# Performance work log

Measured on AMD Instinct MI355X. Metric: run time of the kernel, lower is better.

The kernel has to match this reference:

```python
import jax, jax.numpy as jnp
import numpy as np
import math

B, HR, WR, C = 8, 128, 128, 192
WS, SS = 8, 4
NH, SPH, CHH = 8, 6, 2
DH = C // NH  # 24
AREA = WS * WS
MID = max(C // 4, 8)
NWIN = (HR // WS) * (WR // WS)
LOGMAX = math.log(100.0)

def _rel_pos_index(ws):
    coords = np.stack(np.meshgrid(np.arange(ws), np.arange(ws), indexing='ij')).reshape(2, -1)
    rel = (coords[:, :, None] - coords[:, None, :]).transpose(1, 2, 0).copy()
    rel[:, :, 0] += ws - 1
    rel[:, :, 1] += ws - 1
    rel[:, :, 0] *= 2 * ws - 1
    return rel.sum(-1)  # (AREA, AREA)

def _attn_mask(H, W, ws, ss):
    img = np.zeros((H, W))
    sl = (slice(0, -ws), slice(-ws, -ss), slice(-ss, None))
    cnt = 0
    for hs in sl:
        for wsl in sl:
            img[hs, wsl] = cnt
            cnt += 1
    mw = img.reshape(H // ws, ws, W // ws, ws).transpose(0, 2, 1, 3).reshape(-1, ws * ws)
    am = mw[:, None, :] - mw[:, :, None]
    return np.where(am != 0, -100.0, 0.0).astype(np.float32)

REL_IDX = jnp.asarray(_rel_pos_index(WS))
ATTN_MASK = jnp.asarray(_attn_mask(HR, WR, WS, SS))  # (NWIN, AREA, AREA)

def _norm(v):
    return v / jnp.maximum(jnp.linalg.norm(v, axis=-1, keepdims=True), 1e-12)

def _ln(x, g, b):
    m = x.mean(-1, keepdims=True)
    v = x.var(-1, keepdims=True)
    return (x - m) / jnp.sqrt(v + 1e-5) * g + b

def _bn(x, g, b, m, v):
    return (x - m) / jnp.sqrt(v + 1e-5) * g + b

def _conv3(x, w):  # x: NHWC, w: (O,I,3,3) torch layout
    return jax.lax.conv_general_dilated(x, jnp.transpose(w, (2, 3, 1, 0)), (1, 1), 'SAME', dimension_numbers=('NHWC', 'HWIO', 'NHWC'))

def _forward(x, ln1_g, ln1_b, w_qkv, b_qkv, logit_sp, rpb_table, w_spp, b_spp, logit_ch, w_chp, b_chp, w_sp_proj, w_ch_proj, w_s2c1, w_s2c2, b_s2c2, w_c2s1, w_c2s2, b_c2s2, w_gs1, w_gs2, b_gs2, w_gc1, w_gc2, b_gc2, w_f1, bn1_g, bn1_b, bn1_m, bn1_v, w_f2, bn2_g, bn2_b, bn2_m, bn2_v, w_sg1, w_sg2, b_sg2, ln2_g, ln2_b, w_fc1, b_fc1, w_fc2, b_fc2):
    h = _ln(x, ln1_g, ln1_b)
    img = h.reshape(B, HR, WR, C)
    # qkv conv1x1; per-head channel blocks of 3*DH (faithful to torch view)
    qkv = (img @ w_qkv.T + b_qkv).reshape(B, HR, WR, NH, 3 * DH)
    # ---- spatial shifted-window cosine attention (heads 0:SPH) ----
    sp = jnp.roll(qkv[..., :SPH, :], (-SS, -SS), axis=(1, 2))
    nHw, nWw = HR // WS, WR // WS
    sp = sp.reshape(B, nHw, WS, nWw, WS, SPH, 3 * DH).transpose(0, 1, 3, 5, 2, 4, 6)
    sp = sp.reshape(B * NWIN, SPH, AREA, 3 * DH)
    q, k, v = jnp.split(sp, 3, axis=-1)
    attn = jnp.einsum('bhid,bhjd->bhij', _norm(q), _norm(k))
    attn = attn * jnp.exp(jnp.minimum(logit_sp, LOGMAX)).reshape(1, SPH, 1, 1)
    attn = attn + rpb_table[REL_IDX].transpose(2, 0, 1)[None]
    attn = attn.reshape(B, NWIN, SPH, AREA, AREA) + ATTN_MASK[None, :, None]
    attn = jax.nn.softmax(attn.reshape(B * NWIN, SPH, AREA, AREA), axis=-1)
    o = jnp.einsum('bhij,bhjd->bhid', attn, v)
    o = o.reshape(B, nHw, nWw, SPH, WS, WS, DH).transpose(0, 1, 4, 2, 5, 3, 6).reshape(B, HR, WR, SPH * DH)
    o = o @ w_spp.T + b_spp
    sp_out = jnp.roll(o, (SS, SS), axis=(1, 2)) @ w_sp_proj.T  # (B,H,W,C)
    # ---- channel cosine self-attention (heads SPH:NH) ----
    chq = qkv[..., SPH:, :].reshape(B, HR * WR, CHH, 3 * DH).transpose(0, 2, 3, 1)  # (B,hh,3dh,HW)
    qc, kc, vc = jnp.split(chq, 3, axis=2)
    a = jnp.einsum('bhci,bhdi->bhcd', _norm(qc), _norm(kc))
    a = jax.nn.softmax(a * jnp.exp(jnp.minimum(logit_ch, LOGMAX)).reshape(1, CHH, 1, 1), axis=-1)
    oc = jnp.einsum('bhcd,bhdi->bhci', a, vc).reshape(B, CHH * DH, HR * WR)
    oc = oc.transpose(0, 2, 1).reshape(B, HR, WR, CHH * DH)
    ch_out = (oc @ w_chp.T + b_chp) @ w_ch_proj.T  # (B,H,W,C)
    # ---- CFCA cross gating ----
    def mlp1(t, w1, w2, b2):
        return jax.nn.relu(t @ w1.T) @ w2.T + b2
    sp2ch = mlp1(sp_out, w_s2c1, w_s2c2, b_s2c2) * jax.nn.sigmoid(mlp1(sp_out.mean((1, 2), keepdims=True), w_gs1, w_gs2, b_gs2))
    ch2sp = mlp1(ch_out, w_c2s1, w_c2s2, b_c2s2) * jax.nn.sigmoid(mlp1(ch_out.mean((1, 2), keepdims=True), w_gc1, w_gc2, b_gc2))
    spf = sp_out + ch2sp
    chf = ch_out + sp2ch
    # ---- XFF fusion (BN in eval mode) ----
    f = jnp.concatenate([spf, chf], axis=-1) @ w_f1.T
    f = jax.nn.relu(_bn(f, bn1_g, bn1_b, bn1_m, bn1_v))
    f = jax.nn.relu(_bn(_conv3(f, w_f2), bn2_g, bn2_b, bn2_m, bn2_v))
    g = jax.nn.sigmoid(jax.nn.relu(_conv3(f, w_sg1)) @ w_sg2.T + b_sg2)
    fused = f * g + f
    # ---- transformer block residual + MLP ----
    x = x + fused.reshape(B, HR * WR, C)
    h2 = _ln(x, ln2_g, ln2_b)
    return x + (jax.nn.gelu(h2 @ w_fc1.T + b_fc1, approximate=False) @ w_fc2.T + b_fc2)

def setup_inputs() -> dict:
    keys = iter(jax.random.split(jax.random.key(0), 64))
    def rn(shape, s=0.02):
        return jax.random.normal(next(keys), shape, dtype=jnp.float32) * s
    z = lambda *s: jnp.zeros(s, dtype=jnp.float32)
    o = lambda *s: jnp.ones(s, dtype=jnp.float32)
    return {
        'x': jax.random.normal(next(keys), (B, HR * WR, C), dtype=jnp.float32),
        'ln1_g': o(C), 'ln1_b': z(C),
        'w_qkv': rn((3 * C, C)), 'b_qkv': z(3 * C),
        'logit_sp': jnp.full((SPH,), math.log(10.0), dtype=jnp.float32),
        'rpb_table': rn(((2 * WS - 1) ** 2, SPH)),
        'w_spp': rn((SPH * DH, SPH * DH)), 'b_spp': z(SPH * DH),
        'logit_ch': jnp.full((CHH,), math.log(10.0), dtype=jnp.float32),
        'w_chp': rn((CHH * DH, CHH * DH)), 'b_chp': z(CHH * DH),
        'w_sp_proj': rn((C, SPH * DH)), 'w_ch_proj': rn((C, CHH * DH)),
        'w_s2c1': rn((MID, C)), 'w_s2c2': rn((C, MID)), 'b_s2c2': z(C),
        'w_c2s1': rn((MID, C)), 'w_c2s2': rn((C, MID)), 'b_c2s2': z(C),
        'w_gs1': rn((MID, C)), 'w_gs2': rn((C, MID)), 'b_gs2': z(C),
        'w_gc1': rn((MID, C)), 'w_gc2': rn((C, MID)), 'b_gc2': z(C),
        'w_f1': rn((C, 2 * C)),
        'bn1_g': o(C), 'bn1_b': z(C), 'bn1_m': z(C), 'bn1_v': o(C),
        'w_f2': rn((C, C, 3, 3)),
        'bn2_g': o(C), 'bn2_b': z(C), 'bn2_m': z(C), 'bn2_v': o(C),
        'w_sg1': rn((C // 2, C, 3, 3)), 'w_sg2': rn((1, C // 2)), 'b_sg2': z(1),
        'ln2_g': o(C), 'ln2_b': z(C),
        'w_fc1': rn((4 * C, C)), 'b_fc1': z(4 * C), 'w_fc2': rn((C, 4 * C)), 'b_fc2': z(C),
    }

def reference(x, ln1_g, ln1_b, w_qkv, b_qkv, logit_sp, rpb_table, w_spp, b_spp, logit_ch, w_chp, b_chp, w_sp_proj, w_ch_proj, w_s2c1, w_s2c2, b_s2c2, w_c2s1, w_c2s2, b_c2s2, w_gs1, w_gs2, b_gs2, w_gc1, w_gc2, b_gc2, w_f1, bn1_g, bn1_b, bn1_m, bn1_v, w_f2, bn2_g, bn2_b, bn2_m, bn2_v, w_sg1, w_sg2, b_sg2, ln2_g, ln2_b, w_fc1, b_fc1, w_fc2, b_fc2):
    return _forward(x, ln1_g, ln1_b, w_qkv, b_qkv, logit_sp, rpb_table, w_spp, b_spp, logit_ch, w_chp, b_chp, w_sp_proj, w_ch_proj, w_s2c1, w_s2c2, b_s2c2, w_c2s1, w_c2s2, b_c2s2, w_gs1, w_gs2, b_gs2, w_gc1, w_gc2, b_gc2, w_f1, bn1_g, bn1_b, bn1_m, bn1_v, w_f2, bn2_g, bn2_b, bn2_m, bn2_v, w_sg1, w_sg2, b_sg2, ln2_g, ln2_b, w_fc1, b_fc1, w_fc2, b_fc2)
```

## Files before the change

### kernel.cpp

```cpp
#include <hip/hip_runtime.h>
#include <hip/hip_bf16.h>
#include <cstddef>

typedef __hip_bfloat16 bf16;
typedef unsigned short u16;
typedef unsigned int u32;
typedef short s16x8 __attribute__((ext_vector_type(8)));
typedef float f32x4 __attribute__((ext_vector_type(4)));

#define BATCH 8
#define HR 128
#define WR 128
#define CCH 192
#define HW (HR*WR)
#define MTOK (BATCH*HW)
#define SPH 6
#define SPC 432
#define CHC 144
#define NWIN 256
#define MIDC 48
#define PH 130
#define PHW (PH*PH)
#define LOGMAX 4.6051701859880914f

static const size_t OFF_A0    = 0;
static const size_t OFF_B0    = 113246208;
static const size_t OFF_C0    = 150994944;
static const size_t OFF_SMALL = 188743680;
static const size_t SO_STATS  = 0;
static const size_t SO_PGRAM  = 1048576;
static const size_t SO_PSS    = 1638400;
static const size_t SO_ATTNB  = 1687552;
static const size_t SO_MEANSP = 1724416;
static const size_t SO_MEANCH = 1732608;
static const size_t SO_GATES  = 1740800;
static const size_t SO_GATEC  = 1748992;
static const size_t SO_BCSP   = 1757184;
static const size_t SO_WCCH   = 1758208;
static const size_t SO_BCCH   = 1795072;
static const size_t SO_WFUSE  = 1796096;
static const size_t SO_WCSPB  = 1943552;
static const size_t SO_WQB    = 1998848;
static const size_t SO_WS2C1B = 2220032;
static const size_t SO_WC2S1B = 2238464;
static const size_t SO_WS2C2B = 2256896;
static const size_t SO_WC2S2B = 2275328;
static const size_t SO_WF1B   = 2293760;
static const size_t SO_WF2CB  = 2441216;
static const size_t SO_WSG1CB = 3104768;
static const size_t SO_WFC1B  = 3436544;
static const size_t SO_WFC2B  = 3731456;

__device__ __forceinline__ float b2f(bf16 x) { return __bfloat162float(x); }
__device__ __forceinline__ bf16  f2b(float x){ return __float2bfloat16(x); }
__device__ __forceinline__ u16   f2u(float x){
    bf16 h = __float2bfloat16(x);
    union { bf16 b; u16 u; } c; c.b = h; return c.u;
}
__device__ __forceinline__ float s2f(short s){
    union { u16 u; bf16 b; } c; c.u = (u16)s; return b2f(c.b);
}
__device__ __forceinline__ float u2f(u16 u){
    union { u16 u; bf16 b; } c; c.u = u; return b2f(c.b);
}
__device__ __forceinline__ int xcdswz(int b, int n){
    const int q = n >> 3, r = n & 7, x = b & 7, o = b >> 3;
    return (x < r) ? (x * (q + 1) + o) : (r * (q + 1) + (x - r) * q + o);
}

#define GBM 128
#define GBK 32
#define LDA 40

struct SegRaw { union { uint4 v; struct { float4 lo, hi; } f; } d; };

template<int AMODE, int EPI, int CBF, int BNT, int CPAD, int WPB>
__global__ __launch_bounds__(256)
void gemm_k(const void* __restrict__ A, const u16* __restrict__ W,
            const float* __restrict__ bias, void* __restrict__ Cv,
            int M, int N, int K,
            const float* __restrict__ stats, const float* __restrict__ lng,
            const float* __restrict__ lnb, const void* __restrict__ A2,
            const float* __restrict__ ep0, const float* __restrict__ ep1,
            const float* __restrict__ ep2, const float* __restrict__ ep3)
{
    constexpr int NF = BNT / 32;
    constexpr int NB = (BNT * 4 + 255) / 256;
    constexpr int ATILE = GBM * LDA;
    constexpr int BTILE = BNT * LDA;
    constexpr int BUFSZ = ATILE + BTILE;
    constexpr int CST   = BNT + 8;
    __shared__ __align__(16) u16 smem[2 * BUFSZ];

    const int tid  = threadIdx.x;
    const int lane = tid & 63;
    const int wid  = tid >> 6;
    const int wm   = (wid >> 1) * 64;
    const int wn   = (wid & 1) * (BNT / 2);
    const int m0   = xcdswz(blockIdx.y, gridDim.y) * GBM;
    const int n0   = blockIdx.x * BNT;
    const int row16 = lane & 15;
    const int hi    = lane >> 4;
    const int koff  = hi * 8;

    const int arow[2] = { tid >> 2, (tid + 256) >> 2 };
    const int akk     = (tid & 3) * 8;

    const u16* Wb = W;
    if constexpr (WPB) Wb = W + (size_t)(m0 >> 14) * 9216;

    float meanA[2], rstdA[2];
    if constexpr (AMODE == 1) {
        #pragma unroll
        for (int it = 0; it < 2; ++it) {
            const int m = m0 + arow[it];
            meanA[it] = stats[2*m]; rstdA[it] = stats[2*m+1];
        }
    }

    f32x4 acc[4][NF];
    #pragma unroll
    for (int mf = 0; mf < 4; ++mf)
        #pragma unroll
        for (int nf = 0; nf < NF; ++nf)
            acc[mf][nf] = (f32x4){0.f, 0.f, 0.f, 0.f};

    const int nsteps = (K + GBK - 1) / GBK;

    auto loadA = [&](int step, SegRaw seg[2]) {
        const int k0 = step * GBK;
        #pragma unroll
        for (int it = 0; it < 2; ++it) {
            const int m = m0 + arow[it];
            const int k = k0 + akk;
            SegRaw& s = seg[it];
            if (k >= K) { s.d.v = (uint4){0u,0u,0u,0u}; continue; }
            if constexpr (AMODE == 0) {
                s.d.v = *(const uint4*)((const u16*)A + (size_t)m * K + k);
            } else if constexpr (AMODE == 1) {
                const float* p = (const float*)A + (size_t)m * K + k;
                s.d.f.lo = *(const float4*)p; s.d.f.hi = *(const float4*)(p+4);
            } else if constexpr (AMODE == 2) {
                const u16* src = (k < CCH) ? (const u16*)A  + (size_t)m * CCH + k
                                           : (const u16*)A2 + (size_t)m * CCH + (k - CCH);
                s.d.v = *(const uint4*)src;
            } else if constexpr (AMODE == 3) {
                const int tap = k / CCH, c = k - tap * CCH;
                const int ky = tap / 3, kx = tap - ky * 3;
                const int b = m >> 14, pix = m & 16383;
                const int h = pix >> 7, w = pix & 127;
                s.d.v = *(const uint4*)((const u16*)A +
                        ((size_t)b * PHW + (size_t)(h + ky) * PH + (w + kx)) * CCH + c);
            } else {
                const int col = (k < 24) ? (48 + k) : (96 + k);
                s.d.v = *(const uint4*)((const u16*)A + (size_t)m * CHC + col);
            }
        }
    };
    auto loadB = [&](int step, SegRaw seg[NB]) {
        const int k0 = step * GBK;
        #pragma unroll
        for (int it = 0; it < NB; ++it) {
            const int s = tid + it * 256;
            const int n = n0 + (s >> 2);
            const int k = k0 + (s & 3) * 8;
            seg[it].d.v = (uint4){0u,0u,0u,0u};
            if (s < BNT*4 && k < K && n < N)
                seg[it].d.v = *(const uint4*)(Wb + (size_t)n * K + k);
        }
    };
    auto writeA = [&](int step, SegRaw seg[2], u16* Ab) {
        const int k0 = step * GBK;
        #pragma unroll
        for (int it = 0; it < 2; ++it) {
            if constexpr (AMODE == 1) {
                const int k = k0 + akk;
                union { u16 u[8]; uint4 v; } pk;
                #pragma unroll
                for (int j = 0; j < 8; ++j) {
                    float xx = (j < 4) ? seg[it].d.f.lo[j] : seg[it].d.f.hi[j-4];
                    xx = (xx - meanA[it]) * rstdA[it] * lng[k+j] + lnb[k+j];
                    pk.u[j] = f2u(xx);
                }
                *(uint4*)&Ab[arow[it] * LDA + akk] = pk.v;
            } else {
                *(uint4*)&Ab[arow[it] * LDA + akk] = seg[it].d.v;
            }
        }
    };
    auto writeB = [&](SegRaw seg[NB], u16* Bb) {
        #pragma unroll
        for (int it = 0; it < NB; ++it) {
            const int s = tid + it * 256;
            if (s < BNT*4)
                *(uint4*)&Bb[(s >> 2) * LDA + (s & 3) * 8] = seg[it].d.v;
        }
    };

    SegRaw segA[2], segB[NB];
    loadA(0, segA); loadB(0, segB);
    writeA(0, segA, smem); writeB(segB, smem + ATILE);
    __syncthreads();

    int cur = 0;
    for (int step = 0; step < nsteps; ++step) {
        const bool more = (step + 1 < nsteps);
        if (more) { loadA(step+1, segA); loadB(step+1, segB); }
        u16* Ab = smem + cur * BUFSZ;
        u16* Bb = Ab + ATILE;
        s16x8 af[4], bfr[NF];
        #pragma unroll
        for (int mf = 0; mf < 4; ++mf)
            af[mf] = *(const s16x8*)&Ab[(wm + mf*16 + row16) * LDA + koff];
        #pragma unroll
        for (int nf = 0; nf < NF; ++nf)
            bfr[nf] = *(const s16x8*)&Bb[(wn + nf*16 + row16) * LDA + koff];
        __builtin_amdgcn_s_setprio(1);
        #pragma unroll
        for (int mf = 0; mf < 4; ++mf)
            #pragma unroll
            for (int nf = 0; nf < NF; ++nf)
                acc[mf][nf] = __builtin_amdgcn_mfma_f32_16x16x32_bf16(
                    af[mf], bfr[nf], acc[mf][nf], 0, 0, 0);
        __builtin_amdgcn_s_setprio(0);
        if (more) {
            u16* An = smem + (cur ^ 1) * BUFSZ;
            writeA(step+1, segA, An); writeB(segB, An + ATILE);
        }
        __syncthreads();
        cur ^= 1;
    }

    if constexpr (CBF == 1) {
        #pragma unroll
        for (int mf = 0; mf < 4; ++mf) {
            #pragma unroll
            for (int nf = 0; nf < NF; ++nf) {
                const int n = n0 + wn + nf*16 + row16;
                #pragma unroll
                for (int r = 0; r < 4; ++r) {
                    const int m_loc = wm + mf*16 + hi*4 + r;
                    float v = acc[mf][nf][r];
                    if (n < N) {
                        v += (bias ? bias[n] : 0.f);
                        if constexpr (EPI == 1) {
                            v = fmaxf(v, 0.f);
                        } else if constexpr (EPI == 3) {
                            v = (v - ep2[n]) * rsqrtf(ep3[n] + 1e-5f) * ep0[n] + ep1[n];
                            v = fmaxf(v, 0.f);
                        } else if constexpr (EPI == 4) {
                            const int b = (m0 + m_loc) >> 14;
                            v = v * ep0[b * N + n];
                        } else if constexpr (EPI == 5) {
                            v = 0.5f * v * (1.f + erff(v * 0.70710678118654752f));
                        }
                    }
                    smem[m_loc * CST + (wn + nf*16 + row16)] = f2u(v);
                }
            }
        }
        __syncthreads();
        constexpr int CHUNKS = BNT / 8;
        constexpr int TASKS  = GBM * CHUNKS / 256;
        #pragma unroll
        for (int t2 = 0; t2 < TASKS; ++t2) {
            const int task  = tid + t2 * 256;
            const int rloc  = task / CHUNKS;
            const int chunk = task - rloc * CHUNKS;
            const int m  = m0 + rloc;
            const int nn = n0 + chunk * 8;
            if (nn >= N) continue;
            uint4 val = *(const uint4*)&smem[rloc * CST + chunk * 8];
            if constexpr (EPI == 7) {
                if (nn < SPC) {
                    *(uint4*)((u16*)Cv + (size_t)m * SPC + nn) = val;
                } else {
                    u16* chq = (u16*)ep0;
                    *(uint4*)(chq + (size_t)m * CHC + (nn - SPC)) = val;
                }
                continue;
            }
            size_t outIdx;
            if constexpr (CPAD == 1) {
                const int b = m >> 14, pix = m & 16383;
                const int h = pix >> 7, w = pix & 127;
                outIdx = ((size_t)b * PHW + (size_t)(h+1) * PH + (w+1)) * (size_t)N + nn;
            } else if constexpr (EPI == 2) {
                const int b = m >> 14, pix = m & 16383;
                const int h2 = ((pix >> 7) + 4) & 127;
                const int w2 = ((pix & 127) + 4) & 127;
                outIdx = ((size_t)(b * HW) + h2 * WR + w2) * (size_t)N + nn;
            } else {
                outIdx = (size_t)m * N + nn;
            }
            if constexpr (EPI == 4) {
                union { uint4 v; u16 u[8]; } sv, ov;
                sv.v = val;
                ov.v = *(const uint4*)((const u16*)Cv + outIdx);
                #pragma unroll
                for (int j = 0; j < 8; ++j)
                    sv.u[j] = f2u(u2f(ov.u[j]) + u2f(sv.u[j]));
                *(uint4*)((u16*)Cv + outIdx) = sv.v;
            } else {
                *(uint4*)((u16*)Cv + outIdx) = val;
            }
        }
    } else {
        float* fs = (float*)smem;
        constexpr int FST = BNT + 16;
        #pragma unroll
        for (int q = 0; q < 4; ++q) {
            __syncthreads();
            if ((wid >> 1) == (q >> 1)) {
                #pragma unroll
                for (int mfi = 0; mfi < 2; ++mfi) {
                    const int mf = (q & 1) * 2 + mfi;
                    #pragma unroll
                    for (int nf = 0; nf < NF; ++nf) {
                        const int n = wn + nf*16 + row16;
                        #pragma unroll
                        for (int r = 0; r < 4; ++r) {
                            const int mloc = mfi*16 + hi*4 + r;
                            fs[mloc * FST + n] = acc[mf][nf][r] + (bias ? bias[n0 + n] : 0.f);
                        }
                    }
                }
            }
            __syncthreads();
            const int TOT = 32 * (BNT/4);
            for (int task = tid; task < TOT; task += 256) {
                const int rloc = task / (BNT/4);
                const int cc = (task - rloc*(BNT/4)) * 4;
                const int m = m0 + q*32 + rloc;
                const int nn = n0 + cc;
                if (nn >= N) continue;
                float4 v4 = *(const float4*)&fs[rloc*FST + cc];
                const size_t oi = (size_t)m * N + nn;
                if constexpr (EPI == 6) {
                    const float4 o4 = *(const float4*)&ep0[oi];
                    v4.x += o4.x; v4.y += o4.y; v4.z += o4.z; v4.w += o4.w;
                }
                *(float4*)&((float*)Cv)[oi] = v4;
            }
        }
    }
}

__global__ __launch_bounds__(256)
void wprep_lin_k(const float* __restrict__ in, bf16* __restrict__ outb, int n)
{
    const int i = blockIdx.x * 256 + threadIdx.x;
    if (i < n) outb[i] = f2b(in[i]);
}

__global__ __launch_bounds__(256)
void wprep_conv_k(const float* __restrict__ in, bf16* __restrict__ outb, int total)
{
    const int i = blockIdx.x * 256 + threadIdx.x;
    if (i >= total) return;
    const int n = i / 1728, r = i - n * 1728;
    const int tap = r / CCH, c = r - tap * CCH;
    outb[i] = f2b(in[((size_t)n * CCH + c) * 9 + tap]);
}

__global__ __launch_bounds__(256)
void zb_k(bf16* __restrict__ buf)
{
    const int i = blockIdx.x * 256 + threadIdx.x;
    if (i >= 8 * 516 * 24) return;
    const int chunk = i % 24;
    const int p = (i / 24) % 516;
    const int b = i / (24 * 516);
    int h, w;
    if (p < 130)      { h = 0;   w = p; }
    else if (p < 260) { h = 129; w = p - 130; }
    else { const int q = p - 260; h = 1 + (q >> 1); w = (q & 1) ? 129 : 0; }
    *(uint4*)((u16*)buf + ((size_t)b * PHW + (size_t)h * PH + w) * CCH + chunk * 8)
        = (uint4){0u,0u,0u,0u};
}

__global__ __launch_bounds__(256)
void zerof_k(float* __restrict__ p, int n)
{
    const int i = blockIdx.x * 256 + threadIdx.x;
    if (i < n) p[i] = 0.f;
}

__global__ __launch_bounds__(256)
void ln_stats_k(const float* __restrict__ x, float* __restrict__ stats)
{
    const int tok = blockIdx.x * 4 + (threadIdx.x >> 6);
    const int lane = threadIdx.x & 63;
    const float* r = x + (size_t)tok * CCH;
    float s = 0.f, sq = 0.f;
    for (int c = lane; c < CCH; c += 64) { float v = r[c]; s += v; sq += v*v; }
    for (int m = 1; m < 64; m <<= 1) { s += __shfl_xor(s, m); sq += __shfl_xor(sq, m); }
    if (lane == 0) {
        const float mean = s / (float)CCH;
        const float var = sq / (float)CCH - mean * mean;
        stats[(size_t)tok*2]   = mean;
        stats[(size_t)tok*2+1] = rsqrtf(var + 1e-5f);
    }
}

__global__ __launch_bounds__(384)
void sp_attn_k(const bf16* __restrict__ spqkv, const float* __restrict__ rpb,
               const float* __restrict__ logit_sp, bf16* __restrict__ osp)
{
    const int b    = blockIdx.x >> 8;
    const int win  = blockIdx.x & 255;
    const int wh = win >> 4, ww = win & 15;
    const int head = threadIdx.x >> 6;
    const int lane = threadIdx.x & 63;
    const int row16 = lane & 15;
    const int hi   = lane >> 4;
    const int koff = hi * 8;

    __shared__ float rpbS[1350];
    __shared__ u16 vT[SPH][32][72];

    for (int i = threadIdx.x; i < 1350; i += 384) rpbS[i] = rpb[i];

    const u16* base = (const u16*)spqkv + (size_t)b * HW * SPC;

    s16x8 qf[4], kf[4];
    const int wcol = (ww*8 + (row16 & 7) + 4) & 127;
    #pragma unroll
    for (int t = 0; t < 4; ++t) {
        const int pos = t*16 + row16;
        const int h = (wh*8 + (pos >> 3) + 4) & 127;
        const u16* rowp = base + ((size_t)(h * WR + wcol)) * SPC + head * 72;
        if (koff < 24) {
            qf[t] = *(const s16x8*)(rowp + koff);
            kf[t] = *(const s16x8*)(rowp + 24 + koff);
        } else {
            qf[t] = (s16x8){0,0,0,0,0,0,0,0};
            kf[t] = (s16x8){0,0,0,0,0,0,0,0};
        }
    }

    {
        const int h = (wh*8 + (lane >> 3) + 4) & 127;
        const int w = (ww*8 + (lane & 7) + 4) & 127;
        const u16* vrow = base + ((size_t)(h * WR + w)) * SPC + head * 72 + 48;
        union { uint4 v; u16 u[8]; } seg[3];
        seg[0].v = *(const uint4*)(vrow);
        seg[1].v = *(const uint4*)(vrow + 8);
        seg[2].v = *(const uint4*)(vrow + 16);
        #pragma unroll
        for (int d = 0; d < 24; ++d) vT[head][d][lane] = seg[d>>3].u[d&7];
        #pragma unroll
        for (int d = 24; d < 32; ++d) vT[head][d][lane] = 0;
    }
    __syncthreads();

    float rq[4], rk[4];
    #pragma unroll
    for (int t = 0; t < 4; ++t) {
        float sq = 0.f, sk = 0.f;
        #pragma unroll
        for (int e = 0; e < 8; ++e) {
            const float a = s2f(qf[t][e]); sq += a*a;
            const float c = s2f(kf[t][e]); sk += c*c;
        }
        sq += __shfl_xor(sq, 16); sq += __shfl_xor(sq, 32);
        sk += __shfl_xor(sk, 16); sk += __shfl_xor(sk, 32);
        rq[t] = 1.f / fmaxf(sqrtf(sq), 1e-12f);
        rk[t] = 1.f / fmaxf(sqrtf(sk), 1e-12f);
    }
    const float scale_h = __expf(fminf(logit_sp[head], LOGMAX));

    f32x4 acc[4][4];
    #pragma unroll
    for (int mfk = 0; mfk < 4; ++mfk)
        #pragma unroll
        for (int nfq = 0; nfq < 4; ++nfq)
            acc[mfk][nfq] = (f32x4){0.f,0.f,0.f,0.f};
    #pragma unroll
    for (int mfk = 0; mfk < 4; ++mfk)
        #pragma unroll
        for (int nfq = 0; nfq < 4; ++nfq)
            acc[mfk][nfq] = __builtin_amdgcn_mfma_f32_16x16x32_bf16(
                kf[mfk], qf[nfq], acc[mfk][nfq], 0, 0, 0);

    f32x4 rkj[4];
    #pragma unroll
    for (int mfk = 0; mfk < 4; ++mfk)
        #pragma unroll
        for (int r = 0; r < 4; ++r)
            rkj[mfk][r] = __shfl(rk[mfk], hi*4 + r);

    int ip3[4], iw7[4], labi[4];
    #pragma unroll
    for (int t = 0; t < 4; ++t) {
        const int pos = t*16 + row16;
        ip3[t] = pos >> 3; iw7[t] = pos & 7;
        const int hh = wh*8 + ip3[t], w0 = ww*8 + iw7[t];
        const int rh = hh < 120 ? 0 : (hh < 124 ? 1 : 2);
        const int rw = w0 < 120 ? 0 : (w0 < 124 ? 1 : 2);
        labi[t] = rh*3 + rw;
    }

    #pragma unroll
    for (int mfk = 0; mfk < 4; ++mfk) {
        #pragma unroll
        for (int r = 0; r < 4; ++r) {
            const int j = hi*4 + r + 16*mfk;
            const int jp3 = j >> 3, jw7 = j & 7;
            const int hh = wh*8 + jp3, w0 = ww*8 + jw7;
            const int rh = hh < 120 ? 0 : (hh < 124 ? 1 : 2);
            const int rw = w0 < 120 ? 0 : (w0 < 124 ? 1 : 2);
            const int labj = rh*3 + rw;
            const float rkv = rkj[mfk][r];
            #pragma unroll
            for (int nfq = 0; nfq < 4; ++nfq) {
                float s = acc[mfk][nfq][r] * rq[nfq] * rkv * scale_h;
                s += rpbS[((ip3[nfq]-jp3+7)*15 + (iw7[nfq]-jw7+7))*SPH + head];
                if (labi[nfq] != labj) s -= 100.f;
                acc[mfk][nfq][r] = s;
            }
        }
    }

    float inv[4];
    #pragma unroll
    for (int nfq = 0; nfq < 4; ++nfq) {
        float m = -1e30f;
        #pragma unroll
        for (int mfk = 0; mfk < 4; ++mfk)
            #pragma unroll
            for (int r = 0; r < 4; ++r)
                m = fmaxf(m, acc[mfk][nfq][r]);
        m = fmaxf(m, __shfl_xor(m, 16));
        m = fmaxf(m, __shfl_xor(m, 32));
        float s = 0.f;
        #pragma unroll
        for (int mfk = 0; mfk < 4; ++mfk)
            #pragma unroll
            for (int r = 0; r < 4; ++r) {
                const float p = __expf(acc[mfk][nfq][r] - m);
                acc[mfk][nfq][r] = p;
                s += p;
            }
        s += __shfl_xor(s, 16);
        s += __shfl_xor(s, 32);
        inv[nfq] = 1.f / s;
    }

    u32 pk01[4][4], pk23[4][4];
    #pragma unroll
    for (int mfk = 0; mfk < 4; ++mfk)
        #pragma unroll
        for (int nfq = 0; nfq < 4; ++nfq) {
            pk01[mfk][nfq] = (u32)f2u(acc[mfk][nfq][0] * inv[nfq])
                           | ((u32)f2u(acc[mfk][nfq][1] * inv[nfq]) << 16);
            pk23[mfk][nfq] = (u32)f2u(acc[mfk][nfq][2] * inv[nfq])
                           | ((u32)f2u(acc[mfk][nfq][3] * inv[nfq]) << 16);
        }

    s16x8 vf[2][2];
    #pragma unroll
    for (int nf = 0; nf < 2; ++nf)
        #pragma unroll
        for (int ks = 0; ks < 2; ++ks)
            vf[nf][ks] = *(const s16x8*)&vT[head][row16 + 16*nf][32*ks + koff];

    f32x4 accO[4][2];
    #pragma unroll
    for (int MF = 0; MF < 4; ++MF)
        #pragma unroll
        for (int nf = 0; nf < 2; ++nf)
            accO[MF][nf] = (f32x4){0.f,0.f,0.f,0.f};

    const int g0 = 2*(hi & 1);
    const int src0 = g0*16 + row16, src1 = src0 + 16;
    const bool selhi = (hi >> 1) != 0;
    #pragma unroll
    for (int ks = 0; ks < 2; ++ks) {
        #pragma unroll
        for (int MF = 0; MF < 4; ++MF) {
            const u32 e01a = __shfl(pk01[2*ks][MF],   src0);
            const u32 e01b = __shfl(pk01[2*ks+1][MF], src0);
            const u32 e23a = __shfl(pk23[2*ks][MF],   src0);
            const u32 e23b = __shfl(pk23[2*ks+1][MF], src0);
            const u32 e45a = __shfl(pk01[2*ks][MF],   src1);
            const u32 e45b = __shfl(pk01[2*ks+1][MF], src1);
            const u32 e67a = __shfl(pk23[2*ks][MF],   src1);
            const u32 e67b = __shfl(pk23[2*ks+1][MF], src1);
            union { u32 w[4]; s16x8 v; } af;
            af.w[0] = selhi ? e01b : e01a;
            af.w[1] = selhi ? e23b : e23a;
            af.w[2] = selhi ? e45b : e45a;
            af.w[3] = selhi ? e67b : e67a;
            accO[MF][0] = __builtin_amdgcn_mfma_f32_16x16x32_bf16(
                af.v, vf[0][ks], accO[MF][0], 0, 0, 0);
            accO[MF][1] = __builtin_amdgcn_mfma_f32_16x16x32_bf16(
                af.v, vf[1][ks], accO[MF][1], 0, 0, 0);
        }
    }

    #pragma unroll
    for (int MF = 0; MF < 4; ++MF) {
        #pragma unroll
        for (int nf = 0; nf < 2; ++nf) {
            const int d = row16 + 16*nf;
            if (d >= 24) continue;
            #pragma unroll
            for (int r = 0; r < 4; ++r) {
                const int qrow = hi*4 + r + 16*MF;
                const int h = wh*8 + (qrow >> 3);
                const int w = ww*8 + (qrow & 7);
                osp[((size_t)b*HW + h*WR + w)*144 + head*24 + d] = f2b(accO[MF][nf][r]);
            }
        }
    }
}

__global__ __launch_bounds__(256)
void ch_part_k(const bf16* __restrict__ chqkv, float* __restrict__ pgram,
               float* __restrict__ pss)
{
    const int ci = blockIdx.x, head = blockIdx.y, b = blockIdx.z;
    const int tid = threadIdx.x;
    __shared__ u16 tile[256][48];
    float g[3] = {0.f, 0.f, 0.f};
    float ss = 0.f;
    const u16* src = (const u16*)chqkv + (size_t)b * HW * CHC + head * 72;
    const int rbase = ci * 1024;

    for (int t0 = 0; t0 < 1024; t0 += 256) {
        __syncthreads();
        for (int idx = tid; idx < 256*6; idx += 256) {
            const int row = idx / 6, seg = idx - (idx/6)*6;
            *(uint4*)&tile[row][seg*8] =
                *(const uint4*)(src + (size_t)(rbase + t0 + row) * CHC + seg*8);
        }
        __syncthreads();
        #pragma unroll
        for (int i = 0; i < 3; ++i) {
            const int e = tid + i*256;
            if (e < 576) {
                const int c = e / 24, d = e - (e/24)*24;
                float s = 0.f;
                for (int r = 0; r < 256; ++r)
                    s += b2f(*(const bf16*)&tile[r][c]) * b2f(*(const bf16*)&tile[r][24+d]);
                g[i] += s;
            }
        }
        if (tid < 48) {
            float s = 0.f;
            for (int r = 0; r < 256; ++r) { const float v = b2f(*(const bf16*)&tile[r][tid]); s += v*v; }
            ss += s;
        }
    }
    float* pg = pgram + ((size_t)(b*2+head)*16 + ci) * 576;
    #pragma unroll
    for (int i = 0; i < 3; ++i) { const int e = tid + i*256; if (e < 576) pg[e] = g[i]; }
    if (tid < 48) pss[((size_t)(b*2+head)*16 + ci) * 48 + tid] = ss;
}

__global__ __launch_bounds__(256)
void ch_soft_k(const float* __restrict__ pgram, const float* __restrict__ pss,
               const float* __restrict__ logit_ch, float* __restrict__ attn)
{
    const int head = blockIdx.x, b = blockIdx.y;
    const int tid = threadIdx.x;
    __shared__ float gs[576], rn[48];
    for (int e = tid; e < 576; e += 256) {
        float s = 0.f;
        const float* pg = pgram + (size_t)(b*2+head)*16*576 + e;
        for (int c = 0; c < 16; ++c) s += pg[c*576];
        gs[e] = s;
    }
    if (tid < 48) {
        float s = 0.f;
        const float* ps = pss + (size_t)(b*2+head)*16*48 + tid;
        for (int c = 0; c < 16; ++c) s += ps[c*48];
        rn[tid] = 1.f / fmaxf(sqrtf(s), 1e-12f);
    }
    __syncthreads();
    if (tid < 24) {
        const float scale = expf(fminf(logit_ch[head], LOGMAX));
        float vals[24], mx = -1e30f;
        #pragma unroll
        for (int d = 0; d < 24; ++d) {
            vals[d] = gs[tid*24+d] * rn[tid] * rn[24+d] * scale;
            mx = fmaxf(mx, vals[d]);
        }
        float sum = 0.f;
        #pragma unroll
        for (int d = 0; d < 24; ++d) { vals[d] = expf(vals[d]-mx); sum += vals[d]; }
        const float inv = 1.f / sum;
        float* o = attn + ((size_t)(b*2+head)*24 + tid)*24;
        #pragma unroll
        for (int d = 0; d < 24; ++d) o[d] = vals[d]*inv;
    }
}

__global__ __launch_bounds__(192)
void fuse_chw_k(const float* __restrict__ Wc, const float* __restrict__ attn,
                bf16* __restrict__ Wf)
{
    const int b = blockIdx.x;
    const int n = threadIdx.x;
    __shared__ float As_[2][24][24];
    for (int e = n; e < 1152; e += 192) {
        const int h = e / 576, r = e - h*576;
        As_[h][r/24][r%24] = attn[(size_t)b*1152 + e];
    }
    __syncthreads();
    const float* wr = Wc + n*48;
    bf16* o = Wf + ((size_t)b*192 + n) * 48;
    for (int h = 0; h < 2; ++h)
        for (int d = 0; d < 24; ++d) {
            float s = 0.f;
            #pragma unroll
            for (int cc = 0; cc < 24; ++cc) s += wr[h*24+cc] * As_[h][cc][d];
            o[h*24+d] = f2b(s);
        }
}

__global__ void combine_sp_k(const float* __restrict__ w_sp_proj, const float* __restrict__ w_spp,
                             const float* __restrict__ b_spp, bf16* __restrict__ Wc, float* __restrict__ bc)
{
    const int n = blockIdx.x;
    for (int i = threadIdx.x; i < 144; i += blockDim.x) {
        float s = 0.f;
        for (int j = 0; j < 144; ++j) s += w_sp_proj[n*144 + j] * w_spp[j*144 + i];
        Wc[n*144 + i] = f2b(s);
    }
    if (threadIdx.x == 0) {
        float s = 0.f;
        for (int j = 0; j < 144; ++j) s += w_sp_proj[n*144 + j] * b_spp[j];
        bc[n] = s;
    }
}

__global__ void combine_ch_k(const float* __restrict__ w_ch_proj, const float* __restrict__ w_chp,
                             const float* __restrict__ b_chp, float* __restrict__ Wc, float* __restrict__ bc)
{
    const int n = blockIdx.x;
    for (int c = threadIdx.x; c < 48; c += blockDim.x) {
        float s = 0.f;
        for (int j = 0; j < 48; ++j) s += w_ch_proj[n*48 + j] * w_chp[j*48 + c];
        Wc[n*48 + c] = s;
    }
    if (threadIdx.x == 0) {
        float s = 0.f;
        for (int j = 0; j < 48; ++j) s += w_ch_proj[n*48 + j] * b_chp[j];
        bc[n] = s;
    }
}

__global__ __launch_bounds__(256)
void mean2_k(const bf16* __restrict__ src, float* __restrict__ dst)
{
    const int b = blockIdx.y;
    const int r0 = blockIdx.x * 256;
    const int t = threadIdx.x;
    const int chunk = t & 31;
    const int rg = t >> 5;
    float acc[8] = {0.f,0.f,0.f,0.f,0.f,0.f,0.f,0.f};
    if (chunk < 24) {
        for (int r = rg; r < 256; r += 8) {
            const u16* p = (const u16*)src + ((size_t)(b*HW) + r0 + r) * CCH + chunk*8;
            union { uint4 v; u16 u[8]; } s; s.v = *(const uint4*)p;
            #pragma unroll
            for (int j = 0; j < 8; ++j) acc[j] += u2f(s.u[j]);
        }
    }
    __shared__ float red[8][24][8];
    if (chunk < 24) {
        #pragma unroll
        for (int j = 0; j < 8; ++j) red[rg][chunk][j] = acc[j];
    }
    __syncthreads();
    if (t < 192) {
        const int ch = t >> 3, j = t & 7;
        float s = 0.f;
        #pragma unroll
        for (int g = 0; g < 8; ++g) s += red[g][ch][j];
        atomicAdd(&dst[b*CCH + ch*8 + j], s);
    }
}

__global__ __launch_bounds__(192)
void gates_k(const float* __restrict__ sumv, const float* __restrict__ w1,
             const float* __restrict__ w2, const float* __restrict__ b2,
             float* __restrict__ gate)
{
    const int b = blockIdx.x;
    __shared__ float mv[192], hid[48];
    const int t = threadIdx.x;
    mv[t] = sumv[b*CCH + t] * (1.f / (float)HW);
    __syncthreads();
    if (t < 48) {
        float s = 0.f;
        for (int c = 0; c < 192; ++c) s += w1[t*192 + c] * mv[c];
        hid[t] = fmaxf(s, 0.f);
    }
    __syncthreads();
    float s = b2[t];
    for (int j = 0; j < 48; ++j) s += hid[j] * w2[t*48 + j];
    gate[b*CCH + t] = 1.f / (1.f + expf(-s));
}

__global__ __launch_bounds__(256)
void fuse_k(const float* __restrict__ x, const bf16* __restrict__ f2pad,
            const bf16* __restrict__ gpre, const float* __restrict__ w_sg2,
            const float* __restrict__ b_sg2, float* __restrict__ out)
{
    const int pix = blockIdx.x * 4 + (threadIdx.x >> 6);
    const int lane = threadIdx.x & 63;
    const bf16* gp = gpre + (size_t)pix * 96;
    float s = fmaxf(b2f(gp[lane]), 0.f) * w_sg2[lane];
    if (lane < 32) s += fmaxf(b2f(gp[lane + 64]), 0.f) * w_sg2[lane + 64];
    for (int m = 1; m < 64; m <<= 1) s += __shfl_xor(s, m);
    const float g1 = 1.f + 1.f / (1.f + expf(-(s + b_sg2[0])));
    const int b = pix >> 14, p = pix & 16383;
    const int h = p >> 7, w = p & 127;
    const bf16* fr = f2pad + ((size_t)b * PHW + (size_t)(h+1) * PH + (w+1)) * CCH;
    const float* xr = x + (size_t)pix * CCH;
    float* orow = out + (size_t)pix * CCH;
    for (int c = lane; c < CCH; c += 64) orow[c] = xr[c] + b2f(fr[c]) * g1;
}

extern "C" void kernel_launch(void* const* d_in, const int* in_sizes, int n_in,
                              void* d_out, int out_size, void* d_ws, size_t ws_size,
                              hipStream_t stream)
{
    const float* x        = (const float*)d_in[0];
    const float* ln1_g    = (const float*)d_in[1];
    const float* ln1_b    = (const float*)d_in[2];
    const float* w_qkv    = (const float*)d_in[3];
    const float* b_qkv    = (const float*)d_in[4];
    const float* logit_sp = (const float*)d_in[5];
    const float* rpb      = (const float*)d_in[6];
    const float* w_spp    = (const float*)d_in[7];
    const float* b_spp    = (const float*)d_in[8];
    const float* logit_ch = (const float*)d_in[9];
    const float* w_chp    = (const float*)d_in[10];
    const float* b_chp    = (const float*)d_in[11];
    const float* w_sp_proj= (const float*)d_in[12];
    const float* w_ch_proj= (const float*)d_in[13];
    const float* w_s2c1   = (const float*)d_in[14];
    const float* w_s2c2   = (const float*)d_in[15];
    const float* b_s2c2   = (const float*)d_in[16];
    const float* w_c2s1   = (const float*)d_in[17];
    const float* w_c2s2   = (const float*)d_in[18];
    const float* b_c2s2   = (const float*)d_in[19];
    const float* w_gs1    = (const float*)d_in[20];
    const float* w_gs2    = (const float*)d_in[21];
    const float* b_gs2    = (const float*)d_in[22];
    const float* w_gc1    = (const float*)d_in[23];
    const float* w_gc2    = (const float*)d_in[24];
    const float* b_gc2    = (const float*)d_in[25];
    const float* w_f1     = (const float*)d_in[26];
    const float* bn1_g    = (const float*)d_in[27];
    const float* bn1_b    = (const float*)d_in[28];
    const float* bn1_m    = (const float*)d_in[29];
    const float* bn1_v    = (const float*)d_in[30];
    const float* w_f2     = (const float*)d_in[31];
    const float* bn2_g    = (const float*)d_in[32];
    const float* bn2_b    = (const float*)d_in[33];
    const float* bn2_m    = (const float*)d_in[34];
    const float* bn2_v    = (const float*)d_in[35];
    const float* w_sg1    = (const float*)d_in[36];
    const float* w_sg2    = (const float*)d_in[37];
    const float* b_sg2    = (const float*)d_in[38];
    const float* ln2_g    = (const float*)d_in[39];
    const float* ln2_b    = (const float*)d_in[40];
    const float* w_fc1    = (const float*)d_in[41];
    const float* b_fc1    = (const float*)d_in[42];
    const float* w_fc2    = (const float*)d_in[43];
    const float* b_fc2    = (const float*)d_in[44];

    char* wsb = (char*)d_ws;
    char* sm  = wsb + OFF_SMALL;
    float* out = (float*)d_out;

    bf16*  spqkv  = (bf16*)(wsb + OFF_A0);
    bf16*  sp_out = (bf16*)(wsb + OFF_A0);
    bf16*  ch_out = (bf16*)(wsb + OFF_A0 + 50331648);
    bf16*  f2pad  = (bf16*)(wsb + OFF_A0);
    bf16*  gpre   = (bf16*)(wsb + OFF_A0 + 51916800);
    bf16*  chqkv  = (bf16*)(wsb + OFF_B0);
    bf16*  hid_s  = (bf16*)(wsb + OFF_B0);
    bf16*  hid_c  = (bf16*)(wsb + OFF_B0 + 12582912);
    bf16*  fpad   = (bf16*)(wsb + OFF_B0);
    bf16*  hidden = (bf16*)(wsb + OFF_A0);
    bf16*  osp    = (bf16*)(wsb + OFF_C0);

    float* stats  = (float*)(sm + SO_STATS);
    float* pgram  = (float*)(sm + SO_PGRAM);
    float* pss    = (float*)(sm + SO_PSS);
    float* attn_b = (float*)(sm + SO_ATTNB);
    float* mean_sp= (float*)(sm + SO_MEANSP);
    float* mean_ch= (float*)(sm + SO_MEANCH);
    float* gate_s = (float*)(sm + SO_GATES);
    float* gate_c = (float*)(sm + SO_GATEC);
    float* bc_sp  = (float*)(sm + SO_BCSP);
    float* Wc_ch  = (float*)(sm + SO_WCCH);
    float* bc_ch  = (float*)(sm + SO_BCCH);
    bf16*  Wfuse  = (bf16*)(sm + SO_WFUSE);
    bf16*  Wc_spB = (bf16*)(sm + SO_WCSPB);
    u16*   wqB    = (u16*)(sm + SO_WQB);
    u16*   ws2c1B = (u16*)(sm + SO_WS2C1B);
    u16*   wc2s1B = (u16*)(sm + SO_WC2S1B);
    u16*   ws2c2B = (u16*)(sm + SO_WS2C2B);
    u16*   wc2s2B = (u16*)(sm + SO_WC2S2B);
    u16*   wf1B   = (u16*)(sm + SO_WF1B);
    u16*   wf2cB  = (u16*)(sm + SO_WF2CB);
    u16*   wsg1cB = (u16*)(sm + SO_WSG1CB);
    u16*   wfc1B  = (u16*)(sm + SO_WFC1B);
    u16*   wfc2B  = (u16*)(sm + SO_WFC2B);

    const dim3 blk(256);

    wprep_lin_k<<<(110592+255)/256, blk, 0, stream>>>(w_qkv,  (bf16*)wqB,    110592);
    wprep_lin_k<<<(9216+255)/256,   blk, 0, stream>>>(w_s2c1, (bf16*)ws2c1B, 9216);
    wprep_lin_k<<<(9216+255)/256,   blk, 0, stream>>>(w_c2s1, (bf16*)wc2s1B, 9216);
    wprep_lin_k<<<(9216+255)/256,   blk, 0, stream>>>(w_s2c2, (bf16*)ws2c2B, 9216);
    wprep_lin_k<<<(9216+255)/256,   blk, 0, stream>>>(w_c2s2, (bf16*)wc2s2B, 9216);
    wprep_lin_k<<<(73728+255)/256,  blk, 0, stream>>>(w_f1,   (bf16*)wf1B,   73728);
    wprep_lin_k<<<(147456+255)/256, blk, 0, stream>>>(w_fc1,  (bf16*)wfc1B,  147456);
    wprep_lin_k<<<(147456+255)/256, blk, 0, stream>>>(w_fc2,  (bf16*)wfc2B,  147456);
    wprep_conv_k<<<(331776+255)/256, blk, 0, stream>>>(w_f2,  (bf16*)wf2cB,  331776);
    wprep_conv_k<<<(165888+255)/256, blk, 0, stream>>>(w_sg1, (bf16*)wsg1cB, 165888);
    combine_sp_k<<<192, 128, 0, stream>>>(w_sp_proj, w_spp, b_spp, Wc_spB, bc_sp);
    combine_ch_k<<<192, 64, 0, stream>>>(w_ch_proj, w_chp, b_chp, Wc_ch, bc_ch);
    zerof_k<<<6, blk, 0, stream>>>(mean_sp, 1536);
    zerof_k<<<6, blk, 0, stream>>>(mean_ch, 1536);

    ln_stats_k<<<MTOK/4, blk, 0, stream>>>(x, stats);
    gemm_k<1,7,1,192,0,0><<<dim3(3, MTOK/GBM), blk, 0, stream>>>(
        x, wqB, b_qkv, spqkv, MTOK, 576, CCH,
        stats, ln1_g, ln1_b, nullptr,
        (const float*)chqkv, nullptr, nullptr, nullptr);

    sp_attn_k<<<dim3(BATCH*NWIN), dim3(384), 0, stream>>>(spqkv, rpb, logit_sp, osp);
    gemm_k<0,2,1,192,0,0><<<dim3(1, MTOK/GBM), blk, 0, stream>>>(
        osp, (const u16*)Wc_spB, bc_sp, sp_out, MTOK, CCH, 144,
        nullptr, nullptr, nullptr, nullptr,
        nullptr, nullptr, nullptr, nullptr);

    ch_part_k<<<dim3(16, 2, BATCH), blk, 0, stream>>>(chqkv, pgram, pss);
    ch_soft_k<<<dim3(2, BATCH), blk, 0, stream>>>(pgram, pss, logit_ch, attn_b);
    fuse_chw_k<<<BATCH, 192, 0, stream>>>(Wc_ch, attn_b, Wfuse);
    gemm_k<4,0,1,192,0,1><<<dim3(1, MTOK/GBM), blk, 0, stream>>>(
        chqkv, (const u16*)Wfuse, bc_ch, ch_out, MTOK, CCH, 48,
        nullptr, nullptr, nullptr, nullptr,
        nullptr, nullptr, nullptr, nullptr);

    mean2_k<<<dim3(HW/256, BATCH), blk, 0, stream>>>(sp_out, mean_sp);
    mean2_k<<<dim3(HW/256, BATCH), blk, 0, stream>>>(ch_out, mean_ch);
    gates_k<<<BATCH, 192, 0, stream>>>(mean_sp, w_gs1, w_gs2, b_gs2, gate_s);
    gates_k<<<BATCH, 192, 0, stream>>>(mean_ch, w_gc1, w_gc2, b_gc2, gate_c);

    gemm_k<0,1,1,96,0,0><<<dim3(1, MTOK/GBM), blk, 0, stream>>>(
        sp_out, ws2c1B, nullptr, hid_s, MTOK, MIDC, CCH,
        nullptr, nullptr, nullptr, nullptr, nullptr, nullptr, nullptr, nullptr);
    gemm_k<0,1,1,96,0,0><<<dim3(1, MTOK/GBM), blk, 0, stream>>>(
        ch_out, wc2s1B, nullptr, hid_c, MTOK, MIDC, CCH,
        nullptr, nullptr, nullptr, nullptr, nullptr, nullptr, nullptr, nullptr);
    gemm_k<0,4,1,192,0,0><<<dim3(1, MTOK/GBM), blk, 0, stream>>>(
        hid_s, ws2c2B, b_s2c2, ch_out, MTOK, CCH, MIDC,
        nullptr, nullptr, nullptr, nullptr, gate_s, nullptr, nullptr, nullptr);
    gemm_k<0,4,1,192,0,0><<<dim3(1, MTOK/GBM), blk, 0, stream>>>(
        hid_c, wc2s2B, b_c2s2, sp_out, MTOK, CCH, MIDC,
        nullptr, nullptr, nullptr, nullptr, gate_c, nullptr, nullptr, nullptr);

    zb_k<<<(8*516*24+255)/256, blk, 0, stream>>>(fpad);
    gemm_k<2,3,1,192,1,0><<<dim3(1, MTOK/GBM), blk, 0, stream>>>(
        sp_out, wf1B, nullptr, fpad, MTOK, CCH, 2*CCH,
        nullptr, nullptr, nullptr, ch_out, bn1_g, bn1_b, bn1_m, bn1_v);

    zb_k<<<(8*516*24+255)/256, blk, 0, stream>>>(f2pad);
    gemm_k<3,3,1,192,1,0><<<dim3(1, MTOK/GBM), blk, 0, stream>>>(
        fpad, wf2cB, nullptr, f2pad, MTOK, CCH, 9*CCH,
        nullptr, nullptr, nullptr, nullptr, bn2_g, bn2_b, bn2_m, bn2_v);

    gemm_k<3,0,1,96,0,0><<<dim3(1, MTOK/GBM), blk, 0, stream>>>(
        f2pad, wsg1cB, nullptr, gpre, MTOK, 96, 9*CCH,
        nullptr, nullptr, nullptr, nullptr, nullptr, nullptr, nullptr, nullptr);

    fuse_k<<<MTOK/4, blk, 0, stream>>>(x, f2pad, gpre, w_sg2, b_sg2, out);

    ln_stats_k<<<MTOK/4, blk, 0, stream>>>(out, stats);
    const int CHM = MTOK / 2;
    for (int c0 = 0; c0 < MTOK; c0 += CHM) {
        gemm_k<1,5,1,192,0,0><<<dim3(4, CHM/GBM), blk, 0, stream>>>(
            out + (size_t)c0*CCH, wfc1B, b_fc1, hidden, CHM, 4*CCH, CCH,
            stats + (size_t)c0*2, ln2_g, ln2_b, nullptr,
            nullptr, nullptr, nullptr, nullptr);
        gemm_k<0,6,0,192,0,0><<<dim3(1, CHM/GBM), blk, 0, stream>>>(
            hidden, wfc2B, b_fc2, out + (size_t)c0*CCH, CHM, CCH, 4*CCH,
            nullptr, nullptr, nullptr, nullptr, out + (size_t)c0*CCH,
            nullptr, nullptr, nullptr);
    }
}
```

Before: 1.337 ms.

## Stage GEMM tiles with direct global-to-LDS loads and shrink shared memory

For full K-steps (except the LayerNorm-fused A path), the GEMM now fills shared memory with global_load_lds (16-byte direct global-to-LDS copies) instead of loading into registers and then storing to LDS. LDA padding drops from 40 to 32 to match the contiguous layout these copies need. The bf16 epilogue is split into two 64-row halves so the staging buffer fits a smaller shared allocation. The aim is to cut register pressure and VALU/LDS-store work and to raise occupancy. The risks are LDS bank conflicts from the unpadded stride and possibly missing waits (vmcnt) before the sync.

```diff
diff --git a/kernel.cpp b/kernel.cpp
--- a/kernel.cpp
+++ b/kernel.cpp
@@ -67,10 +67,15 @@
     const int q = n >> 3, r = n & 7, x = b & 7, o = b >> 3;
     return (x < r) ? (x * (q + 1) + o) : (r * (q + 1) + (x - r) * q + o);
 }
+__device__ __forceinline__ void gload16(const void* g, u16* l) {
+    __builtin_amdgcn_global_load_lds(
+        (const __attribute__((address_space(1))) void*)g,
+        (__attribute__((address_space(3))) void*)l, 16, 0, 0);
+}
 
 #define GBM 128
 #define GBK 32
-#define LDA 40
+#define LDA 32
 
 struct SegRaw { union { uint4 v; struct { float4 lo, hi; } f; } d; };
 
@@ -90,7 +95,11 @@
     constexpr int BTILE = BNT * LDA;
     constexpr int BUFSZ = ATILE + BTILE;
     constexpr int CST   = BNT + 8;
-    __shared__ __align__(16) u16 smem[2 * BUFSZ];
+    constexpr int CSTG  = 64 * CST;
+    constexpr int FSTG  = 32 * (BNT + 16) * 2;
+    constexpr int SM1 = (2*BUFSZ > CSTG) ? 2*BUFSZ : CSTG;
+    constexpr int SMEMSZ = (SM1 > FSTG) ? SM1 : FSTG;
+    __shared__ __align__(16) u16 smem[SMEMSZ];
 
     const int tid  = threadIdx.x;
     const int lane = tid & 63;
@@ -127,46 +136,61 @@
 
     const int nsteps = (K + GBK - 1) / GBK;
 
+    auto aAddr = [&](int s, int k0) -> const void* {
+        const int m = m0 + (s >> 2);
+        const int k = k0 + (s & 3) * 8;
+        if constexpr (AMODE == 0) {
+            return (const u16*)A + (size_t)m * K + k;
+        } else if constexpr (AMODE == 2) {
+            return (k < CCH) ? (const void*)((const u16*)A  + (size_t)m * CCH + k)
+                             : (const void*)((const u16*)A2 + (size_t)m * CCH + (k - CCH));
+        } else if constexpr (AMODE == 3) {
+            const int tap = k / CCH, c = k - tap * CCH;
+            const int ky = tap / 3, kx = tap - ky * 3;
+            const int b = m >> 14, pix = m & 16383;
+            const int h = pix >> 7, w = pix & 127;
+            return (const u16*)A + ((size_t)b * PHW + (size_t)(h + ky) * PH + (w + kx)) * CCH + c;
+        } else {
+            const int col = (k < 24) ? (48 + k) : (96 + k);
+            return (const u16*)A + (size_t)m * CHC + col;
+        }
+    };
+
+    auto gstageA = [&](int step, u16* Ab) {
+        const int k0 = step * GBK;
+        #pragma unroll
+        for (int it = 0; it < 2; ++it) {
+            const int s = tid + it * 256;
+            gload16(aAddr(s, k0), &Ab[(it*256 + wid*64) * 8]);
+        }
+    };
+    auto gstageB = [&](int step, u16* Bb) {
+        const int k0 = step * GBK;
+        #pragma unroll
+        for (int it = 0; it < NB; ++it) {
+            const int s = tid + it * 256;
+            if (s < BNT*4) {
+                int n = n0 + (s >> 2);
+                if (n >= N) n = N - 1;
+                gload16(Wb + (size_t)n * K + (k0 + (s & 3) * 8),
+                        &Bb[(it*256 + wid*64) * 8]);
+            }
+        }
+    };
+
     auto loadA = [&](int step, SegRaw seg[2]) {
         const int k0 = step * GBK;
         #pragma unroll
         for (int it = 0; it < 2; ++it) {
-            const int m = m0 + arow[it];
             const int k = k0 + akk;
             SegRaw& s = seg[it];
             if (k >= K) { s.d.v = (uint4){0u,0u,0u,0u}; continue; }
-            if constexpr (AMODE == 0) {
-                s.d.v = *(const uint4*)((const u16*)A + (size_t)m * K + k);
-            } else if constexpr (AMODE == 1) {
-                const float* p = (const float*)A + (size_t)m * K + k;
+            if constexpr (AMODE == 1) {
+                const float* p = (const float*)A + (size_t)(m0 + arow[it]) * K + k;
                 s.d.f.lo = *(const float4*)p; s.d.f.hi = *(const float4*)(p+4);
-            } else if constexpr (AMODE == 2) {
-                const u16* src = (k < CCH) ? (const u16*)A  + (size_t)m * CCH + k
-                                           : (const u16*)A2 + (size_t)m * CCH + (k - CCH);
-                s.d.v = *(const uint4*)src;
-            } else if constexpr (AMODE == 3) {
-                const int tap = k / CCH, c = k - tap * CCH;
-                const int ky = tap / 3, kx = tap - ky * 3;
-                const int b = m >> 14, pix = m & 16383;
-                const int h = pix >> 7, w = pix & 127;
-                s.d.v = *(const uint4*)((const u16*)A +
-                        ((size_t)b * PHW + (size_t)(h + ky) * PH + (w + kx)) * CCH + c);
             } else {
-                const int col = (k < 24) ? (48 + k) : (96 + k);
-                s.d.v = *(const uint4*)((const u16*)A + (size_t)m * CHC + col);
-            }
-        }
-    };
-    auto loadB = [&](int step, SegRaw seg[NB]) {
-        const int k0 = step * GBK;
-        #pragma unroll
-        for (int it = 0; it < NB; ++it) {
-            const int s = tid + it * 256;
-            const int n = n0 + (s >> 2);
-            const int k = k0 + (s & 3) * 8;
-            seg[it].d.v = (uint4){0u,0u,0u,0u};
-            if (s < BNT*4 && k < K && n < N)
-                seg[it].d.v = *(const uint4*)(Wb + (size_t)n * K + k);
+                s.d.v = *(const uint4*)aAddr(it*256 + tid, k0);
+            }
         }
     };
     auto writeA = [&](int step, SegRaw seg[2], u16* Ab) {
@@ -188,6 +212,18 @@
             }
         }
     };
+    auto loadB = [&](int step, SegRaw seg[NB]) {
+        const int k0 = step * GBK;
+        #pragma unroll
+        for (int it = 0; it < NB; ++it) {
+            const int s = tid + it * 256;
+            const int n = n0 + (s >> 2);
+            const int k = k0 + (s & 3) * 8;
+            seg[it].d.v = (uint4){0u,0u,0u,0u};
+            if (s < BNT*4 && k < K && n < N)
+                seg[it].d.v = *(const uint4*)(Wb + (size_t)n * K + k);
+        }
+    };
     auto writeB = [&](SegRaw seg[NB], u16* Bb) {
         #pragma unroll
         for (int it = 0; it < NB; ++it) {
@@ -198,14 +234,37 @@
     };
 
     SegRaw segA[2], segB[NB];
-    loadA(0, segA); loadB(0, segB);
-    writeA(0, segA, smem); writeB(segB, smem + ATILE);
+
+    {
+        u16* Ab = smem; u16* Bb = smem + ATILE;
+        const bool full0 = (GBK <= K);
+        if constexpr (AMODE == 1) {
+            loadA(0, segA); writeA(0, segA, Ab);
+        } else {
+            if (full0) gstageA(0, Ab);
+            else { loadA(0, segA); writeA(0, segA, Ab); }
+        }
+        if (full0) gstageB(0, Bb);
+        else { loadB(0, segB); writeB(segB, Bb); }
+    }
     __syncthreads();
 
     int cur = 0;
     for (int step = 0; step < nsteps; ++step) {
         const bool more = (step + 1 < nsteps);
-        if (more) { loadA(step+1, segA); loadB(step+1, segB); }
+        u16* An = smem + (cur ^ 1) * BUFSZ;
+        u16* Bn = An + ATILE;
+        if (more) {
+            const bool fullN = ((step + 1) * GBK + GBK <= K);
+            if constexpr (AMODE == 1) {
+                loadA(step + 1, segA);
+            } else {
+                if (fullN) gstageA(step + 1, An);
+                else { loadA(step + 1, segA); writeA(step + 1, segA, An); }
+            }
+            if (fullN) gstageB(step + 1, Bn);
+            else { loadB(step + 1, segB); writeB(segB, Bn); }
+        }
         u16* Ab = smem + cur * BUFSZ;
         u16* Bb = Ab + ATILE;
         s16x8 af[4], bfr[NF];
@@ -224,85 +283,88 @@
                     af[mf], bfr[nf], acc[mf][nf], 0, 0, 0);
         __builtin_amdgcn_s_setprio(0);
         if (more) {
-            u16* An = smem + (cur ^ 1) * BUFSZ;
-            writeA(step+1, segA, An); writeB(segB, An + ATILE);
+            if constexpr (AMODE == 1) writeA(step + 1, segA, An);
         }
         __syncthreads();
         cur ^= 1;
     }
 
     if constexpr (CBF == 1) {
-        #pragma unroll
-        for (int mf = 0; mf < 4; ++mf) {
-            #pragma unroll
-            for (int nf = 0; nf < NF; ++nf) {
-                const int n = n0 + wn + nf*16 + row16;
+        constexpr int CHUNKS = BNT / 8;
+        #pragma unroll
+        for (int hh = 0; hh < 2; ++hh) {
+            __syncthreads();
+            if ((wid >> 1) == hh) {
                 #pragma unroll
-                for (int r = 0; r < 4; ++r) {
-                    const int m_loc = wm + mf*16 + hi*4 + r;
-                    float v = acc[mf][nf][r];
-                    if (n < N) {
-                        v += (bias ? bias[n] : 0.f);
-                        if constexpr (EPI == 1) {
-                            v = fmaxf(v, 0.f);
-                        } else if constexpr (EPI == 3) {
-                            v = (v - ep2[n]) * rsqrtf(ep3[n] + 1e-5f) * ep0[n] + ep1[n];
-                            v = fmaxf(v, 0.f);
-                        } else if constexpr (EPI == 4) {
-                            const int b = (m0 + m_loc) >> 14;
-                            v = v * ep0[b * N + n];
-                        } else if constexpr (EPI == 5) {
-                            v = 0.5f * v * (1.f + erff(v * 0.70710678118654752f));
+                for (int mf = 0; mf < 4; ++mf) {
+                    #pragma unroll
+                    for (int nf = 0; nf < NF; ++nf) {
+                        const int n = n0 + wn + nf*16 + row16;
+                        #pragma unroll
+                        for (int r = 0; r < 4; ++r) {
+                            const int mloc = mf*16 + hi*4 + r;
+                            float v = acc[mf][nf][r];
+                            if (n < N) {
+                                v += (bias ? bias[n] : 0.f);
+                                if constexpr (EPI == 1) {
+                                    v = fmaxf(v, 0.f);
+                                } else if constexpr (EPI == 3) {
+                                    v = (v - ep2[n]) * rsqrtf(ep3[n] + 1e-5f) * ep0[n] + ep1[n];
+                                    v = fmaxf(v, 0.f);
+                                } else if constexpr (EPI == 4) {
+                                    const int b = (m0 + hh*64 + mloc) >> 14;
+                                    v = v * ep0[b * N + n];
+                                } else if constexpr (EPI == 5) {
+                                    v = 0.5f * v * (1.f + erff(v * 0.70710678118654752f));
+                                }
+                            }
+                            smem[mloc * CST + (wn + nf*16 + row16)] = f2u(v);
                         }
                     }
-                    smem[m_loc * CST + (wn + nf*16 + row16)] = f2u(v);
                 }
             }
-        }
-        __syncthreads();
-        constexpr int CHUNKS = BNT / 8;
-        constexpr int TASKS  = GBM * CHUNKS / 256;
-        #pragma unroll
-        for (int t2 = 0; t2 < TASKS; ++t2) {
-            const int task  = tid + t2 * 256;
-            const int rloc  = task / CHUNKS;
-            const int chunk = task - rloc * CHUNKS;
-            const int m  = m0 + rloc;
-            const int nn = n0 + chunk * 8;
-            if (nn >= N) continue;
-            uint4 val = *(const uint4*)&smem[rloc * CST + chunk * 8];
-            if constexpr (EPI == 7) {
-                if (nn < SPC) {
-                    *(uint4*)((u16*)Cv + (size_t)m * SPC + nn) = val;
+            __syncthreads();
+            const int TOT = 64 * CHUNKS;
+            for (int task = tid; task < TOT; task += 256) {
+                const int rloc  = task / CHUNKS;
+                const int chunk = task - rloc * CHUNKS;
+                const int m  = m0 + hh*64 + rloc;
+                const int nn = n0 + chunk * 8;
+                if (nn >= N) continue;
+                uint4 val = *(const uint4*)&smem[rloc * CST + chunk * 8];
+                if constexpr (EPI == 7) {
+                    if (nn < SPC) {
+                        *(uint4*)((u16*)Cv + (size_t)m * SPC + nn) = val;
+                    } else {
+                        u16* chq = (u16*)ep0;
+                        *(uint4*)(chq + (size_t)m * CHC + (nn - SPC)) = val;
+                    }
+                    continue;
+                }
+                size_t outIdx;
+                if constexpr (CPAD == 1) {
+                    const int b = m >> 14, pix = m & 16383;
+                    const int h = pix >> 7, w = pix & 127;
+                    outIdx = ((size_t)b * PHW + (size_t)(h+1) * PH + (w+1)) * (size_t)N + nn;
+                } else if constexpr (EPI == 2) {
+                    const int b = m >> 14, pix = m & 16383;
+                    const int h2 = ((pix >> 7) + 4) & 127;
+                    const int w2 = ((pix & 127) + 4) & 127;
+                    outIdx = ((size_t)(b * HW) + h2 * WR + w2) * (size_t)N + nn;
                 } else {
-                    u16* chq = (u16*)ep0;
-                    *(uint4*)(chq + (size_t)m * CHC + (nn - SPC)) = val;
+                    outIdx = (size_t)m * N + nn;
                 }
-                continue;
-            }
-            size_t outIdx;
-            if constexpr (CPAD == 1) {
-                const int b = m >> 14, pix = m & 16383;
-                const int h = pix >> 7, w = pix & 127;
-                outIdx = ((size_t)b * PHW + (size_t)(h+1) * PH + (w+1)) * (size_t)N + nn;
-            } else if constexpr (EPI == 2) {
-                const int b = m >> 14, pix = m & 16383;
-                const int h2 = ((pix >> 7) + 4) & 127;
-                const int w2 = ((pix & 127) + 4) & 127;
-                outIdx = ((size_t)(b * HW) + h2 * WR + w2) * (size_t)N + nn;
-            } else {
-                outIdx = (size_t)m * N + nn;
-            }
-            if constexpr (EPI == 4) {
-                union { uint4 v; u16 u[8]; } sv, ov;
-                sv.v = val;
-                ov.v = *(const uint4*)((const u16*)Cv + outIdx);
-                #pragma unroll
-                for (int j = 0; j < 8; ++j)
-                    sv.u[j] = f2u(u2f(ov.u[j]) + u2f(sv.u[j]));
-                *(uint4*)((u16*)Cv + outIdx) = sv.v;
-            } else {
-                *(uint4*)((u16*)Cv + outIdx) = val;
+                if constexpr (EPI == 4) {
+                    union { uint4 v; u16 u[8]; } sv, ov;
+                    sv.v = val;
+                    ov.v = *(const uint4*)((const u16*)Cv + outIdx);
+                    #pragma unroll
+                    for (int j = 0; j < 8; ++j)
+                        sv.u[j] = f2u(u2f(ov.u[j]) + u2f(sv.u[j]));
+                    *(uint4*)((u16*)Cv + outIdx) = sv.v;
+                } else {
+                    *(uint4*)((u16*)Cv + outIdx) = val;
+                }
             }
         }
     } else {
```

After: 1.653 ms. +23.6%, slower.
